# Kernel optimization log

Hardware: AMD Instinct MI355X
Metric: run time of the kernel (lower is better)

The kernel has to match this reference:

```python
import jax, jax.numpy as jnp
import numpy as np

B, T, N, H = 256, 512, 128, 128  # batch, timesteps(l), num_classes, num_hidden


def setup_inputs() -> dict:
    key = jax.random.key(0)
    ks = jax.random.split(key, 7)
    s = 0.05
    return {
        "x": jax.random.normal(ks[0], (B, T, N), dtype=jnp.float32),
        "Wf": jax.random.normal(ks[1], (N, 4 * H), dtype=jnp.float32) * s,
        "Uf": jax.random.normal(ks[2], (H, 4 * H), dtype=jnp.float32) * s,
        "bf": jax.random.normal(ks[3], (4 * H,), dtype=jnp.float32) * s,
        "Wb": jax.random.normal(ks[4], (N, 4 * H), dtype=jnp.float32) * s,
        "Ub": jax.random.normal(ks[5], (H, 4 * H), dtype=jnp.float32) * s,
        "bb": jax.random.normal(ks[6], (4 * H,), dtype=jnp.float32) * s,
    }


def _lstm_scan(xs, W, U, b):
    # xs: [T, B, N]; Keras gate order i, f, g(c), o. Zero initial state.
    def step(carry, xt):
        h, c = carry
        z = xt @ W + h @ U + b  # [B, 4H]
        i, f, g, o = jnp.split(z, 4, axis=-1)
        i = jax.nn.sigmoid(i)
        f = jax.nn.sigmoid(f)
        g = jnp.tanh(g)
        o = jax.nn.sigmoid(o)
        c = f * c + i * g
        h = o * jnp.tanh(c)
        return (h, c), h

    h0 = jnp.zeros((xs.shape[1], U.shape[0]), dtype=xs.dtype)
    c0 = jnp.zeros_like(h0)
    _, hs = jax.lax.scan(step, (h0, c0), xs)
    return hs  # [T, B, H]


def reference(x, Wf, Uf, bf, Wb, Ub, bb):
    xs = jnp.transpose(x, (1, 0, 2))  # [T, B, N]
    f_hs = _lstm_scan(xs, Wf, Uf, bf)            # forward over t = 0..T-1
    b_hs = _lstm_scan(xs[::-1], Wb, Ub, bb)      # backward cell over reversed seq
    # Original code stacks concat(f_h_i, b_h_i) at loop index i WITHOUT
    # re-reversing the backward stream, so we concat step-aligned streams.
    out = jnp.concatenate([f_hs, b_hs], axis=-1)  # [T, B, 2H]
    return jnp.transpose(out, (1, 0, 2))  # [B, T, 2H]
```

## Files before the change

kernel.cpp:

```cpp
#include <hip/hip_runtime.h>


typedef short s16x8 __attribute__((ext_vector_type(8)));
typedef float f32x4 __attribute__((ext_vector_type(4)));

#define NT 512
#define LDSROW 264

#define LDS_BARRIER() asm volatile("s_waitcnt lgkmcnt(0)\n\ts_barrier" ::: "memory")

__device__ __forceinline__ unsigned short f2bf(float f) {
  unsigned int u = __float_as_uint(f);
  u += 0x7fffu + ((u >> 16) & 1u);
  return (unsigned short)(u >> 16);
}
__device__ __forceinline__ float sigm(float x) {
  return __builtin_amdgcn_rcpf(1.f + __expf(-x));
}
__device__ __forceinline__ float tanh_(float x) {
  float xc = fminf(fmaxf(x, -12.f), 12.f);
  return 1.f - 2.f * __builtin_amdgcn_rcpf(1.f + __expf(2.f * xc));
}

__global__ void prep_frags(const float* __restrict__ Wf, const float* __restrict__ Uf,
                           const float* __restrict__ Wb, const float* __restrict__ Ub,
                           unsigned short* __restrict__ frag) {
  int idx = blockIdx.x * 256 + threadIdx.x;
  int j    = idx & 7;
  int lane = (idx >> 3) & 63;
  int tile = (idx >> 9) & 7;
  int kc   = (idx >> 12) & 7;
  int gate = (idx >> 15) & 3;
  int dir  = (idx >> 17) & 1;
  const float* M = (kc < 4) ? (dir ? Wb : Wf) : (dir ? Ub : Uf);
  int k   = (kc & 3) * 32 + (lane >> 4) * 8 + j;
  int col = gate * 128 + tile * 16 + (lane & 15);
  frag[idx] = f2bf(M[k * 512 + col]);
}

__global__ __launch_bounds__(512, 2) void bilstm_rec(
    const unsigned short* __restrict__ frag, const float* __restrict__ x,
    const float* __restrict__ bfw, const float* __restrict__ bbw,
    float* __restrict__ out) {
  __shared__ unsigned short xh[2][16][LDSROW];

  int bid = blockIdx.x;
  int bblk = bid & 63, dir = bid >> 6;
  int tid = threadIdx.x;
  int tc = tid >> 6, lane = tid & 63, quad = lane >> 4, m = lane & 15;
  bool mrow = ((m & 3) == 0);

  s16x8 wu[4][8];
#pragma unroll
  for (int g = 0; g < 4; g++)
#pragma unroll
    for (int kc = 0; kc < 8; kc++)
      wu[g][kc] = *(const s16x8*)(frag +
          ((((size_t)(dir * 4 + g) * 8 + kc) * 8 + tc) * 64 + lane) * 8);

  const float* bias = dir ? bbw : bfw;
  float bv[4];
#pragma unroll
  for (int g = 0; g < 4; g++) bv[g] = bias[g * 128 + tc * 16 + m];

  int srow = tid >> 7, scol = tid & 127;
  const float* xsrc = x + ((size_t)(bblk * 4 + srow) * NT) * 128 + scol;

  {
    unsigned int* zp = (unsigned int*)&xh[0][0][0];
    for (int i = tid; i < 2 * 16 * (LDSROW / 2); i += 512) zp[i] = 0;
  }
  __syncthreads();

  {
    int t0 = dir ? (NT - 1) : 0;
    xh[0][srow * 4][scol] = f2bf(xsrc[(size_t)t0 * 128]);
  }
  float vxA = xsrc[(size_t)(dir ? (NT - 2) : 1) * 128];
  float vxB = xsrc[(size_t)(dir ? (NT - 3) : 2) * 128];
  __syncthreads();

  s16x8 a[8];
#pragma unroll
  for (int kc = 0; kc < 8; kc++) a[kc] = (s16x8){0, 0, 0, 0, 0, 0, 0, 0};

  float cc = 0.f;
  float* outp = out + ((size_t)(bblk * 4 + quad) * NT) * 256 + dir * 128 + tc * 16 + m;

  auto body = [&](int s, float& vx) {
    int cb = s & 1, nb = cb ^ 1;

    int sn = s + 3; if (sn > NT - 1) sn = NT - 1;
    int tn = dir ? (NT - 1 - sn) : sn;
    float vnew = xsrc[(size_t)tn * 128];

    if (mrow) {
#pragma unroll
      for (int kc = 0; kc < 8; kc++)
        a[kc] = *(const s16x8*)(&xh[cb][m][kc * 32 + quad * 8]);
    }

    f32x4 acc[4];
#pragma unroll
    for (int g = 0; g < 4; g++) {
      acc[g][0] = bv[g]; acc[g][1] = bv[g]; acc[g][2] = bv[g]; acc[g][3] = bv[g];
    }
#pragma unroll
    for (int kc = 0; kc < 8; kc++)
#pragma unroll
      for (int g = 0; g < 4; g++)
        acc[g] = __builtin_amdgcn_mfma_f32_16x16x32_bf16(a[kc], wu[g][kc], acc[g], 0, 0, 0);

    float iv = sigm(acc[0][0]);
    float fv = sigm(acc[1][0]);
    float gv = tanh_(acc[2][0]);
    float ov = sigm(acc[3][0]);
    cc = fv * cc + iv * gv;
    float hv = ov * tanh_(cc);

    xh[nb][quad * 4][128 + tc * 16 + m] = f2bf(hv);
    xh[nb][srow * 4][scol] = f2bf(vx);

    outp[(size_t)s * 256] = hv;

    LDS_BARRIER();
    vx = vnew;
  };

  for (int s = 0; s < NT; s += 2) {
    body(s, vxA);
    body(s + 1, vxB);
  }
}

extern "C" void kernel_launch(void* const* d_in, const int* in_sizes, int n_in,
                              void* d_out, int out_size, void* d_ws, size_t ws_size,
                              hipStream_t stream) {
  const float* x  = (const float*)d_in[0];
  const float* Wf = (const float*)d_in[1];
  const float* Uf = (const float*)d_in[2];
  const float* bf = (const float*)d_in[3];
  const float* Wb = (const float*)d_in[4];
  const float* Ub = (const float*)d_in[5];
  const float* bb = (const float*)d_in[6];
  float* out = (float*)d_out;

  unsigned short* frag = (unsigned short*)d_ws;

  prep_frags<<<1024, 256, 0, stream>>>(Wf, Uf, Wb, Ub, frag);
  bilstm_rec<<<128, 512, 0, stream>>>(frag, x, bf, bb, out);
}
```

Baseline: 492.7 us.

## Hoist input projection into a separate GEMM and slim the recurrent kernel

Splits the x@W input projection out of the sequential LSTM loop into a parallel batched GEMM that writes the pre-activations to a workspace buffer. The recurrent kernel then only multiplies the hidden state by U, halving the MFMA chain per step and reading precomputed gate inputs with a two-step prefetch. This trades a shorter serial critical path for a large extra global-memory round trip through a roughly half-gigabyte buffer, and falls back to the fused kernel if the workspace is too small.

```diff
diff --git a/kernel.cpp b/kernel.cpp
--- a/kernel.cpp
+++ b/kernel.cpp
@@ -13,6 +13,9 @@
   unsigned int u = __float_as_uint(f);
   u += 0x7fffu + ((u >> 16) & 1u);
   return (unsigned short)(u >> 16);
+}
+__device__ __forceinline__ unsigned int packbf2(float a, float b) {
+  return (unsigned int)f2bf(a) | ((unsigned int)f2bf(b) << 16);
 }
 __device__ __forceinline__ float sigm(float x) {
   return __builtin_amdgcn_rcpf(1.f + __expf(-x));
@@ -38,7 +41,168 @@
   frag[idx] = f2bf(M[k * 512 + col]);
 }
 
-__global__ __launch_bounds__(512, 2) void bilstm_rec(
+__global__ __launch_bounds__(512, 2) void zx_gemm(
+    const unsigned short* __restrict__ frag, const float* __restrict__ x,
+    const float* __restrict__ bfw, const float* __restrict__ bbw,
+    float* __restrict__ zx) {
+  __shared__ unsigned short xs[64][136];
+
+  int bid = blockIdx.x;
+  int tile = bid & 2047, dir = bid >> 11;
+  int tid = threadIdx.x;
+  int tc = tid >> 6, lane = tid & 63, quad = lane >> 4, m = lane & 15;
+
+  const float* xt = x + (size_t)tile * (64 * 128);
+#pragma unroll
+  for (int k = 0; k < 4; k++) {
+    int fi = tid + k * 512;
+    int row = fi >> 5, col = (fi & 31) * 4;
+    float4 v = *(const float4*)(xt + row * 128 + col);
+    uint2 pk; pk.x = packbf2(v.x, v.y); pk.y = packbf2(v.z, v.w);
+    *(uint2*)(&xs[row][col]) = pk;
+  }
+
+  s16x8 wu[4][4];
+#pragma unroll
+  for (int g = 0; g < 4; g++)
+#pragma unroll
+    for (int kc = 0; kc < 4; kc++)
+      wu[g][kc] = *(const s16x8*)(frag +
+          ((((size_t)(dir * 4 + g) * 8 + kc) * 8 + tc) * 64 + lane) * 8);
+
+  const float* bias = dir ? bbw : bfw;
+  float bv[4];
+#pragma unroll
+  for (int g = 0; g < 4; g++) bv[g] = bias[g * 128 + tc * 16 + m];
+
+  __syncthreads();
+
+  f32x4 acc[4][4];
+#pragma unroll
+  for (int mt = 0; mt < 4; mt++)
+#pragma unroll
+    for (int g = 0; g < 4; g++) {
+      acc[mt][g][0] = bv[g]; acc[mt][g][1] = bv[g];
+      acc[mt][g][2] = bv[g]; acc[mt][g][3] = bv[g];
+    }
+
+#pragma unroll
+  for (int mt = 0; mt < 4; mt++) {
+    s16x8 a[4];
+#pragma unroll
+    for (int kc = 0; kc < 4; kc++)
+      a[kc] = *(const s16x8*)(&xs[mt * 16 + m][kc * 32 + quad * 8]);
+#pragma unroll
+    for (int kc = 0; kc < 4; kc++)
+#pragma unroll
+      for (int g = 0; g < 4; g++)
+        acc[mt][g] = __builtin_amdgcn_mfma_f32_16x16x32_bf16(a[kc], wu[g][kc], acc[mt][g], 0, 0, 0);
+  }
+
+  float* zo = zx + (size_t)dir * ((size_t)131072 * 512) + (size_t)tile * (64 * 512);
+#pragma unroll
+  for (int mt = 0; mt < 4; mt++)
+#pragma unroll
+    for (int g = 0; g < 4; g++)
+#pragma unroll
+      for (int r = 0; r < 4; r++)
+        zo[(size_t)(mt * 16 + quad * 4 + r) * 512 + g * 128 + tc * 16 + m] = acc[mt][g][r];
+}
+
+__global__ __launch_bounds__(512, 2) void bilstm_rec_lite(
+    const unsigned short* __restrict__ frag, const float* __restrict__ zx,
+    float* __restrict__ out) {
+  __shared__ unsigned short hbuf[2][16][136];
+
+  int bid = blockIdx.x;
+  int bblk = bid & 63, dir = bid >> 6;
+  int tid = threadIdx.x;
+  int tc = tid >> 6, lane = tid & 63, quad = lane >> 4, m = lane & 15;
+  bool mrow = ((m & 3) == 0);
+
+  s16x8 wu[4][4];
+#pragma unroll
+  for (int g = 0; g < 4; g++)
+#pragma unroll
+    for (int kk = 0; kk < 4; kk++)
+      wu[g][kk] = *(const s16x8*)(frag +
+          ((((size_t)(dir * 4 + g) * 8 + 4 + kk) * 8 + tc) * 64 + lane) * 8);
+
+  const float* zp = zx + ((size_t)dir * 131072 + (size_t)(bblk * 4 + quad) * 512) * 512
+                  + tc * 16 + m;
+
+  {
+    unsigned int* zpp = (unsigned int*)&hbuf[0][0][0];
+    for (int i = tid; i < 2 * 16 * 68; i += 512) zpp[i] = 0;
+  }
+  __syncthreads();
+
+  float zqA[4], zqB[4];
+  {
+    int t0 = dir ? (NT - 1) : 0;
+    int t1 = dir ? (NT - 2) : 1;
+#pragma unroll
+    for (int g = 0; g < 4; g++) zqA[g] = zp[(size_t)t0 * 512 + g * 128];
+#pragma unroll
+    for (int g = 0; g < 4; g++) zqB[g] = zp[(size_t)t1 * 512 + g * 128];
+  }
+
+  s16x8 a[4];
+#pragma unroll
+  for (int kk = 0; kk < 4; kk++) a[kk] = (s16x8){0, 0, 0, 0, 0, 0, 0, 0};
+
+  float cc = 0.f;
+  float* outp = out + ((size_t)(bblk * 4 + quad) * NT) * 256 + dir * 128 + tc * 16 + m;
+
+  auto body = [&](int s, float (&zq)[4]) {
+    int cb = s & 1, nb = cb ^ 1;
+
+    int sn = s + 2; if (sn > NT - 1) sn = NT - 1;
+    int tn = dir ? (NT - 1 - sn) : sn;
+    float zn[4];
+#pragma unroll
+    for (int g = 0; g < 4; g++) zn[g] = zp[(size_t)tn * 512 + g * 128];
+
+    if (mrow) {
+#pragma unroll
+      for (int kk = 0; kk < 4; kk++)
+        a[kk] = *(const s16x8*)(&hbuf[cb][m][kk * 32 + quad * 8]);
+    }
+
+    f32x4 acc[4];
+#pragma unroll
+    for (int g = 0; g < 4; g++) {
+      acc[g][0] = zq[g]; acc[g][1] = zq[g]; acc[g][2] = zq[g]; acc[g][3] = zq[g];
+    }
+#pragma unroll
+    for (int kk = 0; kk < 4; kk++)
+#pragma unroll
+      for (int g = 0; g < 4; g++)
+        acc[g] = __builtin_amdgcn_mfma_f32_16x16x32_bf16(a[kk], wu[g][kk], acc[g], 0, 0, 0);
+
+    float iv = sigm(acc[0][0]);
+    float fv = sigm(acc[1][0]);
+    float gv = tanh_(acc[2][0]);
+    float ov = sigm(acc[3][0]);
+    cc = fv * cc + iv * gv;
+    float hv = ov * tanh_(cc);
+
+    hbuf[nb][quad * 4][tc * 16 + m] = f2bf(hv);
+
+    outp[(size_t)s * 256] = hv;
+
+    LDS_BARRIER();
+#pragma unroll
+    for (int g = 0; g < 4; g++) zq[g] = zn[g];
+  };
+
+  for (int s = 0; s < NT; s += 2) {
+    body(s, zqA);
+    body(s + 1, zqB);
+  }
+}
+
+__global__ __launch_bounds__(512, 2) void bilstm_rec_fused(
     const unsigned short* __restrict__ frag, const float* __restrict__ x,
     const float* __restrict__ bfw, const float* __restrict__ bbw,
     float* __restrict__ out) {
@@ -146,7 +310,16 @@
   float* out = (float*)d_out;
 
   unsigned short* frag = (unsigned short*)d_ws;
+  const size_t FRAG_BYTES = 512 * 1024;
+  const size_t ZX_BYTES = (size_t)2 * 131072 * 512 * sizeof(float);
 
   prep_frags<<<1024, 256, 0, stream>>>(Wf, Uf, Wb, Ub, frag);
-  bilstm_rec<<<128, 512, 0, stream>>>(frag, x, bf, bb, out);
-}
+
+  if (ws_size >= FRAG_BYTES + ZX_BYTES) {
+    float* zx = (float*)((char*)d_ws + FRAG_BYTES);
+    zx_gemm<<<4096, 512, 0, stream>>>(frag, x, bf, bb, zx);
+    bilstm_rec_lite<<<128, 512, 0, stream>>>(frag, zx, out);
+  } else {
+    bilstm_rec_fused<<<128, 512, 0, stream>>>(frag, x, bf, bb, out);
+  }
+}
```

Result: no change. 494.5 us (+0.4%).

## Precompute next step's input projection off the recurrent critical path

Applied to the files above, without the earlier changes.

Splits each step's gate GEMM into the recurrent h@U part and the input x@W part. The x@W product for step s+1 is computed during step s into a second accumulator set, so only the h-dependent MFMAs sit on the serial dependency chain. The x prefetch now runs one step further ahead and the LDS x slot holds the next step's input. This adds 16 accumulator registers and reworks the buffer indexing, which may pressure occupancy at launch bounds of 2 blocks.

```diff
diff --git a/kernel.cpp b/kernel.cpp
--- a/kernel.cpp
+++ b/kernel.cpp
@@ -66,55 +66,81 @@
   int srow = tid >> 7, scol = tid & 127;
   const float* xsrc = x + ((size_t)(bblk * 4 + srow) * NT) * 128 + scol;
 
+  auto tmap = [&](int s) { int ss = s > NT - 1 ? NT - 1 : s; return dir ? (NT - 1 - ss) : ss; };
+
   {
     unsigned int* zp = (unsigned int*)&xh[0][0][0];
     for (int i = tid; i < 2 * 16 * (LDSROW / 2); i += 512) zp[i] = 0;
   }
+
+  float vxA = xsrc[(size_t)tmap(2) * 128];
+  float vxB = xsrc[(size_t)tmap(3) * 128];
+
+  float vx1 = xsrc[(size_t)tmap(1) * 128];
+  float vx0 = xsrc[(size_t)tmap(0) * 128];
+  xh[0][srow * 4][scol] = f2bf(vx1);
+  xh[1][srow * 4][scol] = f2bf(vx0);
   __syncthreads();
 
-  {
-    int t0 = dir ? (NT - 1) : 0;
-    xh[0][srow * 4][scol] = f2bf(xsrc[(size_t)t0 * 128]);
+  s16x8 ah[4], ax[4];
+#pragma unroll
+  for (int kk = 0; kk < 4; kk++) { ah[kk] = (s16x8){0,0,0,0,0,0,0,0}; ax[kk] = (s16x8){0,0,0,0,0,0,0,0}; }
+
+  if (mrow) {
+#pragma unroll
+    for (int kk = 0; kk < 4; kk++)
+      ax[kk] = *(const s16x8*)(&xh[1][m][kk * 32 + quad * 8]);
   }
-  float vxA = xsrc[(size_t)(dir ? (NT - 2) : 1) * 128];
-  float vxB = xsrc[(size_t)(dir ? (NT - 3) : 2) * 128];
   __syncthreads();
 
-  s16x8 a[8];
+  f32x4 accA[4], accB[4];
 #pragma unroll
-  for (int kc = 0; kc < 8; kc++) a[kc] = (s16x8){0, 0, 0, 0, 0, 0, 0, 0};
+  for (int g = 0; g < 4; g++) {
+    accA[g][0] = bv[g]; accA[g][1] = bv[g]; accA[g][2] = bv[g]; accA[g][3] = bv[g];
+  }
+#pragma unroll
+  for (int kk = 0; kk < 4; kk++)
+#pragma unroll
+    for (int g = 0; g < 4; g++)
+      accA[g] = __builtin_amdgcn_mfma_f32_16x16x32_bf16(ax[kk], wu[g][kk], accA[g], 0, 0, 0);
 
   float cc = 0.f;
   float* outp = out + ((size_t)(bblk * 4 + quad) * NT) * 256 + dir * 128 + tc * 16 + m;
 
-  auto body = [&](int s, float& vx) {
+  auto body = [&](int s, float& vx, f32x4 (&accC)[4], f32x4 (&accN)[4]) {
     int cb = s & 1, nb = cb ^ 1;
 
-    int sn = s + 3; if (sn > NT - 1) sn = NT - 1;
-    int tn = dir ? (NT - 1 - sn) : sn;
-    float vnew = xsrc[(size_t)tn * 128];
+    float vnew = xsrc[(size_t)tmap(s + 4) * 128];
 
     if (mrow) {
 #pragma unroll
-      for (int kc = 0; kc < 8; kc++)
-        a[kc] = *(const s16x8*)(&xh[cb][m][kc * 32 + quad * 8]);
+      for (int kk = 0; kk < 4; kk++)
+        ah[kk] = *(const s16x8*)(&xh[cb][m][128 + kk * 32 + quad * 8]);
+#pragma unroll
+      for (int kk = 0; kk < 4; kk++)
+        ax[kk] = *(const s16x8*)(&xh[cb][m][kk * 32 + quad * 8]);
     }
 
-    f32x4 acc[4];
+#pragma unroll
+    for (int kk = 0; kk < 4; kk++)
+#pragma unroll
+      for (int g = 0; g < 4; g++)
+        accC[g] = __builtin_amdgcn_mfma_f32_16x16x32_bf16(ah[kk], wu[g][4 + kk], accC[g], 0, 0, 0);
+
 #pragma unroll
     for (int g = 0; g < 4; g++) {
-      acc[g][0] = bv[g]; acc[g][1] = bv[g]; acc[g][2] = bv[g]; acc[g][3] = bv[g];
+      accN[g][0] = bv[g]; accN[g][1] = bv[g]; accN[g][2] = bv[g]; accN[g][3] = bv[g];
     }
 #pragma unroll
-    for (int kc = 0; kc < 8; kc++)
+    for (int kk = 0; kk < 4; kk++)
 #pragma unroll
       for (int g = 0; g < 4; g++)
-        acc[g] = __builtin_amdgcn_mfma_f32_16x16x32_bf16(a[kc], wu[g][kc], acc[g], 0, 0, 0);
+        accN[g] = __builtin_amdgcn_mfma_f32_16x16x32_bf16(ax[kk], wu[g][kk], accN[g], 0, 0, 0);
 
-    float iv = sigm(acc[0][0]);
-    float fv = sigm(acc[1][0]);
-    float gv = tanh_(acc[2][0]);
-    float ov = sigm(acc[3][0]);
+    float iv = sigm(accC[0][0]);
+    float fv = sigm(accC[1][0]);
+    float gv = tanh_(accC[2][0]);
+    float ov = sigm(accC[3][0]);
     cc = fv * cc + iv * gv;
     float hv = ov * tanh_(cc);
 
@@ -128,8 +154,8 @@
   };
 
   for (int s = 0; s < NT; s += 2) {
-    body(s, vxA);
-    body(s + 1, vxB);
+    body(s, vxA, accA, accB);
+    body(s + 1, vxB, accB, accA);
   }
 }
 
```

New measurement: 473.0 us. -4.0%, faster.
